# Performance work log

Hardware: AMD Instinct MI355X
Metric: run time of the kernel (lower is better)

Reference implementation:

```python
import jax, jax.numpy as jnp
import numpy as np

DIM = 2240; HEADS = 20; HD = 112
B = 1; F = 8; H = 16; W = 28; S = F * H * W; ENC = 300
HID = int(3.0 * DIM)  # 6720
EPS_LN = 1e-6; EPS_RMS = 1e-5


def setup_inputs():
    ks = iter(jax.random.split(jax.random.key(0), 64))
    nrm = lambda shape, s=1.0: jax.random.normal(next(ks), shape, jnp.float32) * s
    wsc = 0.02
    inp = dict(
        hidden_states=nrm((B, S, DIM)),
        encoder_hidden_states=nrm((B, ENC, DIM)),
        timestep=nrm((B, 6 * DIM), 0.1),
        freqs_cos=nrm((1, S, 1, HD)),
        freqs_sin=nrm((1, S, 1, HD)),
        scale_shift_table=nrm((6, DIM), 1.0 / np.sqrt(DIM)),
    )
    for p in ("a1", "a2"):
        inp[p + "_qw"] = nrm((DIM, DIM), wsc); inp[p + "_qb"] = jnp.zeros((DIM,), jnp.float32)
        inp[p + "_kw"] = nrm((DIM, DIM), wsc); inp[p + "_kb"] = jnp.zeros((DIM,), jnp.float32)
        inp[p + "_vw"] = nrm((DIM, DIM), wsc); inp[p + "_vb"] = jnp.zeros((DIM,), jnp.float32)
        inp[p + "_nq"] = jnp.ones((DIM,), jnp.float32)
        inp[p + "_nk"] = jnp.ones((DIM,), jnp.float32)
        inp[p + "_ow"] = nrm((DIM, DIM), wsc); inp[p + "_ob"] = jnp.zeros((DIM,), jnp.float32)
    inp["ff_inv_w"] = nrm((1, 1, DIM, 2 * HID), wsc)
    inp["ff_inv_b"] = jnp.zeros((2 * HID,), jnp.float32)
    inp["ff_depth_w"] = nrm((3, 3, 1, 2 * HID), wsc)
    inp["ff_depth_b"] = jnp.zeros((2 * HID,), jnp.float32)
    inp["ff_point_w"] = nrm((1, 1, HID, DIM), wsc)
    inp["ff_temp_w"] = nrm((3, 1, DIM, DIM), wsc)
    inp["frames"] = F; inp["height"] = H; inp["width"] = W
    return inp


def _ln(x):  # LayerNorm, no affine (elementwise_affine=False)
    m = jnp.mean(x, -1, keepdims=True)
    v = jnp.mean((x - m) ** 2, -1, keepdims=True)
    return (x - m) * jax.lax.rsqrt(v + EPS_LN)


def _rms(x, w):  # rms_norm_across_heads on full inner dim
    return x * jax.lax.rsqrt(jnp.mean(x * x, -1, keepdims=True) + EPS_RMS) * w


def _rope(x, cos, sin):  # interleaved rotary as in SanaLinearAttnProcessor3_0
    x1, x2 = x[..., 0::2], x[..., 1::2]
    c, s = cos[..., 0::2], sin[..., 1::2]
    out = jnp.stack([x1 * c - x2 * s, x1 * s + x2 * c], axis=-1)
    return out.reshape(x.shape)


def _conv(x, k, padding, groups=1):
    return jax.lax.conv_general_dilated(
        x, k, (1, 1), padding,
        dimension_numbers=("NHWC", "HWIO", "NHWC"),
        feature_group_count=groups)


def _linear_attn(x, qw, qb, kw, kb, vw, vb, nq, nk, ow, ob, cos, sin):
    b, s, _ = x.shape
    q = jax.nn.relu(_rms(x @ qw + qb, nq)).reshape(b, s, HEADS, HD)
    k = jax.nn.relu(_rms(x @ kw + kb, nk)).reshape(b, s, HEADS, HD)
    v = (x @ vw + vb).reshape(b, s, HEADS, HD)
    qr, kr = _rope(q, cos, sin), _rope(k, cos, sin)
    ksum = jnp.sum(k, axis=1)                             # [b,h,d] (un-rotated)
    denom = jnp.einsum("bhd,bshd->bsh", ksum, q) + 1e-15  # z^{-1}
    scores = jnp.einsum("bshe,bshd->bhed", v, kr)         # [b,h,dv,d]
    out = jnp.einsum("bhed,bshd->bshe", scores, qr) / denom[..., None]
    return out.reshape(b, s, HEADS * HD) @ ow + ob


def _cross_attn(x, enc, qw, qb, kw, kb, vw, vb, nq, nk, ow, ob):
    b, s, _ = x.shape; t = enc.shape[1]
    q = _rms(x @ qw + qb, nq).reshape(b, s, HEADS, HD)
    k = _rms(enc @ kw + kb, nk).reshape(b, t, HEADS, HD)
    v = (enc @ vw + vb).reshape(b, t, HEADS, HD)
    logits = jnp.einsum("bshd,bthd->bhst", q, k) / np.sqrt(HD).astype(np.float32)
    attn = jax.nn.softmax(logits, axis=-1)
    out = jnp.einsum("bhst,bthd->bshd", attn, v).reshape(b, s, HEADS * HD)
    return out @ ow + ob


def _ff(x, inv_w, inv_b, depth_w, depth_b, point_w, temp_w, f, h, w):
    b = x.shape[0]
    y = x.reshape(b * f, h, w, DIM)
    y = jax.nn.silu(_conv(y, inv_w, "SAME") + inv_b)
    y = _conv(y, depth_w, "SAME", groups=2 * HID) + depth_b
    a, g = y[..., :HID], y[..., HID:]
    y = _conv(a * jax.nn.silu(g), point_w, "SAME")        # [bf,h,w,DIM]
    yt = y.reshape(b, f, h * w, DIM)                      # conv over frames axis
    yt = yt + _conv(yt, temp_w, ((1, 1), (0, 0)))
    return yt.reshape(b, f, h, w, DIM)


def reference(hidden_states, encoder_hidden_states, timestep, freqs_cos, freqs_sin,
              scale_shift_table,
              a1_qw, a1_qb, a1_kw, a1_kb, a1_vw, a1_vb, a1_nq, a1_nk, a1_ow, a1_ob,
              a2_qw, a2_qb, a2_kw, a2_kb, a2_vw, a2_vb, a2_nq, a2_nk, a2_ow, a2_ob,
              ff_inv_w, ff_inv_b, ff_depth_w, ff_depth_b, ff_point_w, ff_temp_w,
              frames, height, width):
    b = hidden_states.shape[0]
    mods = scale_shift_table[None] + timestep.reshape(b, 6, DIM)
    sh_msa, sc_msa, g_msa, sh_mlp, sc_mlp, g_mlp = jnp.split(mods, 6, axis=1)
    nh = _ln(hidden_states) * (1 + sc_msa) + sh_msa
    attn = _linear_attn(nh, a1_qw, a1_qb, a1_kw, a1_kb, a1_vw, a1_vb,
                        a1_nq, a1_nk, a1_ow, a1_ob, freqs_cos, freqs_sin)
    x = hidden_states + g_msa * attn
    x = x + _cross_attn(x, encoder_hidden_states, a2_qw, a2_qb, a2_kw, a2_kb,
                        a2_vw, a2_vb, a2_nq, a2_nk, a2_ow, a2_ob)
    nh = _ln(x) * (1 + sc_mlp) + sh_mlp
    ff = _ff(nh.reshape(b, frames, height, width, DIM),
             ff_inv_w, ff_inv_b, ff_depth_w, ff_depth_b, ff_point_w, ff_temp_w,
             frames, height, width)
    x = x + g_mlp * ff.reshape(b, frames * height * width, DIM)
    return x
```

## Files before the change

kernel.cpp:

```cpp
#include <hip/hip_runtime.h>

#define DIMC 2240
#define STOK 3584
#define ENCT 300
#define NH   20
#define HDIM 112
#define HID1 6720
#define HID2 13440
#define DD   (2240*2240)
#define SD   (3584*2240)

typedef short bf16x8 __attribute__((ext_vector_type(8)));
typedef float f32x4  __attribute__((ext_vector_type(4)));

__device__ __forceinline__ unsigned short f2bf(float f){
  unsigned int u = __float_as_uint(f);
  u += 0x7fffu + ((u >> 16) & 1u);
  return (unsigned short)(u >> 16);
}
__device__ __forceinline__ float bf2f(unsigned short h){
  return __uint_as_float(((unsigned int)h) << 16);
}
__device__ __forceinline__ void gl_lds16(const unsigned short* g, unsigned short* l){
  __builtin_amdgcn_global_load_lds(
      (const __attribute__((address_space(1))) unsigned int*)(const void*)g,
      (__attribute__((address_space(3))) unsigned int*)(void*)l, 16, 0, 0);
}

__global__ void cvt_k(const float4* __restrict__ src, ushort4* __restrict__ dst, int n4){
  int i = blockIdx.x*256 + threadIdx.x;
  if (i < n4){
    float4 v = src[i];
    ushort4 o; o.x = f2bf(v.x); o.y = f2bf(v.y); o.z = f2bf(v.z); o.w = f2bf(v.w);
    dst[i] = o;
  }
}

__global__ __launch_bounds__(256) void cvt_t_k(const float* __restrict__ src,
    unsigned short* __restrict__ dst, int rows, int ldsrc, int c0, int nc){
  __shared__ float tile[32][33];
  const int tx = threadIdx.x & 31, ty = threadIdx.x >> 5;
  const int colBase = blockIdx.x*32;
  #pragma unroll
  for (int i = 0; i < 4; ++i){
    int rr = blockIdx.y*32 + ty + i*8;
    int cc = colBase + tx;
    tile[ty + i*8][tx] = (cc < nc) ? src[(size_t)rr*ldsrc + c0 + cc] : 0.f;
  }
  __syncthreads();
  #pragma unroll
  for (int i = 0; i < 4; ++i){
    int n = colBase + ty + i*8;
    int k = blockIdx.y*32 + tx;
    dst[(size_t)n*rows + k] = f2bf(tile[tx][ty + i*8]);
  }
}

__global__ void pack3_k(float* __restrict__ dst, const float* __restrict__ b0,
    const float* __restrict__ b1, const float* __restrict__ b2, int nslots){
  int i = blockIdx.x*256 + threadIdx.x;
  if (i >= nslots*2304) return;
  int slot = i / 2304, d = i - slot*2304;
  const float* src = (slot == 0) ? b0 : ((slot == 1) ? b1 : b2);
  dst[i] = (d < 2240) ? src[d] : 0.f;
}

__global__ void mods_k(const float* __restrict__ sst, const float* __restrict__ ts, float* __restrict__ mods){
  int i = blockIdx.x*256 + threadIdx.x;
  if (i < 6*DIMC) mods[i] = sst[i] + ts[i];
}

__global__ __launch_bounds__(256) void ln_mod_k(const float* __restrict__ x,
    const float* __restrict__ mods, int shj, int scj, unsigned short* __restrict__ out)
{
  const int s = blockIdx.x;
  const float4* row4 = reinterpret_cast<const float4*>(x + (size_t)s*DIMC);
  const float4* sh4 = reinterpret_cast<const float4*>(mods + shj*DIMC);
  const float4* sc4 = reinterpret_cast<const float4*>(mods + scj*DIMC);
  float sum = 0.f, sq = 0.f;
  for (int o = threadIdx.x; o < 560; o += 256){
    float4 v = row4[o];
    sum += v.x + v.y + v.z + v.w;
    sq  += v.x*v.x + v.y*v.y + v.z*v.z + v.w*v.w;
  }
  #pragma unroll
  for (int o = 32; o; o >>= 1){ sum += __shfl_down(sum, o); sq += __shfl_down(sq, o); }
  __shared__ float sA[4], sB[4];
  int w = threadIdx.x >> 6, l = threadIdx.x & 63;
  if (!l){ sA[w] = sum; sB[w] = sq; }
  __syncthreads();
  sum = sA[0]+sA[1]+sA[2]+sA[3];
  sq  = sB[0]+sB[1]+sB[2]+sB[3];
  float mean = sum * (1.f/DIMC);
  float rs = rsqrtf(sq*(1.f/DIMC) - mean*mean + 1e-6f);
  unsigned short* orow = out + (size_t)s*DIMC;
  for (int o = threadIdx.x; o < 560; o += 256){
    float4 v = row4[o], sc = sc4[o], sh = sh4[o];
    ushort4 r;
    r.x = f2bf((v.x-mean)*rs*(1.f + sc.x) + sh.x);
    r.y = f2bf((v.y-mean)*rs*(1.f + sc.y) + sh.y);
    r.z = f2bf((v.z-mean)*rs*(1.f + sc.z) + sh.z);
    r.w = f2bf((v.w-mean)*rs*(1.f + sc.w) + sh.w);
    *reinterpret_cast<ushort4*>(orow + o*4) = r;
  }
}

template<int RELU, int ROPE>
__global__ __launch_bounds__(256) void rms_bf_k(unsigned short* __restrict__ x, const float* __restrict__ nw,
    const float* __restrict__ cosb, const float* __restrict__ sinb, unsigned short* __restrict__ xr)
{
  const int s = blockIdx.x;
  unsigned short* row = x + (size_t)s*DIMC;
  float sq = 0.f;
  for (int o = threadIdx.x; o < 280; o += 256){
    uint4 v = *reinterpret_cast<const uint4*>(row + o*8);
    unsigned int uu[4] = {v.x, v.y, v.z, v.w};
    #pragma unroll
    for (int j = 0; j < 4; ++j){
      float lo = bf2f((unsigned short)(uu[j] & 0xffffu));
      float hi = bf2f((unsigned short)(uu[j] >> 16));
      sq += lo*lo + hi*hi;
    }
  }
  #pragma unroll
  for (int o = 32; o; o >>= 1) sq += __shfl_down(sq, o);
  __shared__ float sB[4];
  int w = threadIdx.x >> 6, l = threadIdx.x & 63;
  if (!l) sB[w] = sq;
  __syncthreads();
  sq = sB[0]+sB[1]+sB[2]+sB[3];
  float rs = rsqrtf(sq*(1.f/DIMC) + 1e-5f);
  for (int o = threadIdx.x; o < 280; o += 256){
    uint4 v = *reinterpret_cast<const uint4*>(row + o*8);
    unsigned int uu[4] = {v.x, v.y, v.z, v.w};
    float4 n0 = *reinterpret_cast<const float4*>(nw + o*8);
    float4 n1 = *reinterpret_cast<const float4*>(nw + o*8 + 4);
    float nn[8] = {n0.x,n0.y,n0.z,n0.w,n1.x,n1.y,n1.z,n1.w};
    float vals[8];
    #pragma unroll
    for (int j = 0; j < 4; ++j){
      vals[2*j]   = bf2f((unsigned short)(uu[j] & 0xffffu))*rs*nn[2*j];
      vals[2*j+1] = bf2f((unsigned short)(uu[j] >> 16))*rs*nn[2*j+1];
    }
    if constexpr (RELU){
      #pragma unroll
      for (int j = 0; j < 8; ++j) vals[j] = fmaxf(vals[j], 0.f);
    }
    uint4 o1;
    unsigned int* po = &o1.x;
    #pragma unroll
    for (int j = 0; j < 4; ++j)
      po[j] = (unsigned int)f2bf(vals[2*j]) | ((unsigned int)f2bf(vals[2*j+1]) << 16);
    *reinterpret_cast<uint4*>(row + o*8) = o1;
    if constexpr (ROPE){
      int jb = (o*8) % HDIM;
      uint4 o2;
      unsigned int* pr = &o2.x;
      #pragma unroll
      for (int p = 0; p < 4; ++p){
        float c  = cosb[(size_t)s*HDIM + jb + 2*p];
        float sn = sinb[(size_t)s*HDIM + jb + 2*p + 1];
        float r0 = vals[2*p]*c - vals[2*p+1]*sn;
        float r1 = vals[2*p]*sn + vals[2*p+1]*c;
        pr[p] = (unsigned int)f2bf(r0) | ((unsigned int)f2bf(r1) << 16);
      }
      *reinterpret_cast<uint4*>(xr + (size_t)s*DIMC + o*8) = o2;
    }
  }
}

template<int EPI>
__global__ __launch_bounds__(256) void gemm_bt(
  const unsigned short* __restrict__ A, const unsigned short* __restrict__ Bt,
  const float* __restrict__ bias, float* __restrict__ Cf, unsigned short* __restrict__ Cb,
  const float* __restrict__ res, const float* __restrict__ gate,
  int M, int N, int K, int ldc, int PW)
{
  __shared__ __align__(16) unsigned short Al[128*64];
  __shared__ __align__(16) unsigned short Bl[128*64];
  const int gx = gridDim.x, gy = gridDim.y;
  const int nwg = gx*gy;
  const int orig = blockIdx.y*gx + blockIdx.x;
  const int qq = nwg >> 3, rr = nwg & 7;
  const int xcd = orig & 7, li = orig >> 3;
  const int wg = (xcd < rr ? xcd*(qq+1) : rr*(qq+1) + (xcd-rr)*qq) + li;
  const int ppw = gy*PW;
  const int panel = wg / ppw, rm = wg - panel*ppw;
  const int mrow = rm / PW;
  const int m0 = mrow*128;
  const int n0 = (panel*PW + (rm - mrow*PW))*128;

  const int t = threadIdx.x, lane = t & 63, w = t >> 6;
  const int wr = w >> 1, wc = w & 1;
  const int l16 = lane & 15, lk = lane >> 4;

  const int lr8 = lane >> 3;
  const int sc  = (lane & 7) ^ lr8;
  const unsigned short* Aps[4];
  const unsigned short* Bps[4];
  #pragma unroll
  for (int i = 0; i < 4; ++i){
    int ar = m0 + w*32 + i*8 + lr8;
    int br = n0 + w*32 + i*8 + lr8;
    Aps[i] = A  + (size_t)min(ar, M-1)*K + sc*8;
    Bps[i] = Bt + (size_t)br*K + sc*8;
  }
  unsigned short* Ad = Al + w*2048;
  unsigned short* Bd = Bl + w*2048;

  f32x4 acc[4][4] = {};
  for (int k0 = 0; k0 < K; k0 += 64){
    __syncthreads();
    #pragma unroll
    for (int i = 0; i < 4; ++i){
      gl_lds16(Aps[i] + k0, Ad + i*512);
      gl_lds16(Bps[i] + k0, Bd + i*512);
    }
    __syncthreads();
    #pragma unroll
    for (int kk = 0; kk < 2; ++kk){
      bf16x8 af[4], bfr[4];
      const int chb = (kk*4 + lk) ^ (l16 & 7);
      #pragma unroll
      for (int m = 0; m < 4; ++m)
        af[m] = *reinterpret_cast<const bf16x8*>(Al + (wr*64 + m*16 + l16)*64 + chb*8);
      #pragma unroll
      for (int n = 0; n < 4; ++n)
        bfr[n] = *reinterpret_cast<const bf16x8*>(Bl + (wc*64 + n*16 + l16)*64 + chb*8);
      #pragma unroll
      for (int m = 0; m < 4; ++m)
        #pragma unroll
        for (int n = 0; n < 4; ++n)
          acc[m][n] = __builtin_amdgcn_mfma_f32_16x16x32_bf16(af[m], bfr[n], acc[m][n], 0, 0, 0);
    }
  }

  const int rb = m0 + wr*64 + lk*4;
  const int cb = n0 + wc*64 + l16;
  #pragma unroll
  for (int m = 0; m < 4; ++m){
    #pragma unroll
    for (int r = 0; r < 4; ++r){
      int row = rb + m*16 + r;
      if (row >= M) continue;
      #pragma unroll
      for (int n = 0; n < 4; ++n){
        int col = cb + n*16;
        if (col >= N) continue;
        float v = acc[m][n][r];
        float bv = bias ? bias[col] : 0.f;
        if constexpr (EPI == 6){
          int slot = col / 2304;
          int d = col - slot*2304;
          if (d < 2240)
            Cb[(size_t)slot*ldc + (size_t)row*2240 + d] = f2bf(v + bv);
        } else {
          size_t idx = (size_t)row*ldc + col;
          if constexpr (EPI == 0){ Cf[idx] = v + bv; }
          else if constexpr (EPI == 1){ float u = v + bv; Cb[idx] = f2bf(u / (1.f + __expf(-u))); }
          else if constexpr (EPI == 2){ Cb[idx] = f2bf(v + bv); }
          else if constexpr (EPI == 3){ float u = res[idx] + gate[col]*(v + bv); Cf[idx] = u; Cb[idx] = f2bf(u); }
          else if constexpr (EPI == 4){ Cf[idx] = res[idx] + v + bv; }
          else { Cf[idx] += v; }
        }
      }
    }
  }
}

__global__ void colsum_k(const unsigned short* __restrict__ k, float* __restrict__ kpart){
  int d = blockIdx.x*256 + threadIdx.x;
  if (d >= DIMC) return;
  int ch = blockIdx.y, s0 = ch*128;
  float acc = 0.f;
  for (int s = s0; s < s0+128; ++s) acc += bf2f(k[(size_t)s*DIMC + d]);
  kpart[(size_t)ch*DIMC + d] = acc;
}
__global__ void ksumred_k(const float* __restrict__ kpart, float* __restrict__ ksum){
  int d = blockIdx.x*256 + threadIdx.x;
  if (d >= DIMC) return;
  float a = 0.f;
  for (int c = 0; c < 28; ++c) a += kpart[(size_t)c*DIMC + d];
  ksum[d] = a;
}
__global__ __launch_bounds__(256) void denom_k(const unsigned short* __restrict__ q,
    const float* __restrict__ ksum, float* __restrict__ denom)
{
  int s = blockIdx.x; int w = threadIdx.x >> 6, l = threadIdx.x & 63;
  for (int h = w; h < NH; h += 4){
    const unsigned short* qb = q + (size_t)s*DIMC + h*HDIM;
    const float* kb = ksum + h*HDIM;
    float v = bf2f(qb[l])*kb[l];
    if (l < 48) v += bf2f(qb[64+l])*kb[64+l];
    #pragma unroll
    for (int o = 32; o; o >>= 1) v += __shfl_down(v, o);
    if (!l) denom[s*NH + h] = v + 1e-15f;
  }
}

#define SLSC 136
__device__ __forceinline__ int sc_idx(int e, int s){
  return e*SLSC + (s ^ (((e >> 3) & 7) << 3));
}
__global__ __launch_bounds__(256) void scores_k(const unsigned short* __restrict__ v,
    const unsigned short* __restrict__ kr, float* __restrict__ part)
{
  const int h = blockIdx.x, ch = blockIdx.y;
  __shared__ __align__(16) unsigned short Vt[112*SLSC];
  __shared__ __align__(16) unsigned short Kt[112*SLSC];
  const int t = threadIdx.x, lane = t & 63, w = t >> 6;
  const int l16 = lane & 15, lk = lane >> 4;
  const int sbase = ch*128;

  for (int p = t; p < 1792; p += 256){
    int s = p / 14, oc = (p % 14) * 8;
    bf16x8 vv = *reinterpret_cast<const bf16x8*>(v  + (size_t)(sbase+s)*DIMC + h*HDIM + oc);
    bf16x8 kk = *reinterpret_cast<const bf16x8*>(kr + (size_t)(sbase+s)*DIMC + h*HDIM + oc);
    #pragma unroll
    for (int j = 0; j < 8; ++j){
      Vt[sc_idx(oc+j, s)] = (unsigned short)vv[j];
      Kt[sc_idx(oc+j, s)] = (unsigned short)kk[j];
    }
  }
  __syncthreads();

  f32x4 acc[2][7] = {};
  #pragma unroll
  for (int ks = 0; ks < 4; ++ks){
    const int sf = ks*32 + lk*8;
    bf16x8 bfrg[7];
    #pragma unroll
    for (int nt = 0; nt < 7; ++nt){
      int d = nt*16 + l16;
      bfrg[nt] = *reinterpret_cast<const bf16x8*>(&Kt[d*SLSC + (sf ^ (((d >> 3) & 7) << 3))]);
    }
    #pragma unroll
    for (int mi = 0; mi < 2; ++mi){
      int mt = w + mi*4;
      if (mt < 7){
        int e = mt*16 + l16;
        bf16x8 afrg = *reinterpret_cast<const bf16x8*>(&Vt[e*SLSC + (sf ^ (((e >> 3) & 7) << 3))]);
        #pragma unroll
        for (int nt = 0; nt < 7; ++nt)
          acc[mi][nt] = __builtin_amdgcn_mfma_f32_16x16x32_bf16(afrg, bfrg[nt], acc[mi][nt], 0, 0, 0);
      }
    }
  }

  float* pout = part + ((size_t)ch*NH + h)*12544;
  #pragma unroll
  for (int mi = 0; mi < 2; ++mi){
    int mt = w + mi*4;
    if (mt >= 7) continue;
    #pragma unroll
    for (int nt = 0; nt < 7; ++nt)
      #pragma unroll
      for (int r = 0; r < 4; ++r)
        pout[(size_t)(mt*16 + lk*4 + r)*HDIM + nt*16 + l16] = acc[mi][nt][r];
  }
}
__global__ void scred_k(const float* __restrict__ part, unsigned short* __restrict__ sc){
  int i = blockIdx.x*256 + threadIdx.x;
  if (i >= NH*HDIM*HDIM) return;
  float a = 0.f;
  #pragma unroll
  for (int c = 0; c < 28; ++c) a += part[(size_t)c*(NH*HDIM*HDIM) + i];
  sc[i] = f2bf(a);
}

__global__ __launch_bounds__(256) void linout_k(const unsigned short* __restrict__ qr,
    const unsigned short* __restrict__ scores, const float* __restrict__ denom,
    unsigned short* __restrict__ out)
{
  const int h = blockIdx.y;
  const int t = threadIdx.x, lane = t & 63, w = t >> 6;
  const int l16 = lane & 15, lk = lane >> 4;
  const int s0 = blockIdx.x*64 + w*16;
  const unsigned short* qrow = qr + (size_t)(s0 + l16)*DIMC + h*HDIM;
  const unsigned short* sb = scores + (size_t)h*12544;
  f32x4 acc[7] = {};
  #pragma unroll
  for (int ks = 0; ks < 4; ++ks){
    int d0 = ks*32 + lk*8;
    bf16x8 a = {};
    if (d0 < HDIM) a = *reinterpret_cast<const bf16x8*>(qrow + d0);
    #pragma unroll
    for (int nt = 0; nt < 7; ++nt){
      bf16x8 b = {};
      if (d0 < HDIM) b = *reinterpret_cast<const bf16x8*>(sb + (size_t)(nt*16 + l16)*HDIM + d0);
      acc[nt] = __builtin_amdgcn_mfma_f32_16x16x32_bf16(a, b, acc[nt], 0, 0, 0);
    }
  }
  #pragma unroll
  for (int r = 0; r < 4; ++r){
    int s = s0 + lk*4 + r;
    float dn = 1.f / denom[(size_t)s*NH + h];
    #pragma unroll
    for (int nt = 0; nt < 7; ++nt)
      out[(size_t)s*DIMC + h*HDIM + nt*16 + l16] = f2bf(acc[nt][r]*dn);
  }
}

__global__ __launch_bounds__(256) void xattn_k(
    const unsigned short* __restrict__ q,
    const unsigned short* __restrict__ k2,
    const unsigned short* __restrict__ v2,
    unsigned short* __restrict__ outb)
{
  const int h = blockIdx.y;
  const int w = threadIdx.x >> 6, lane = threadIdx.x & 63;
  const int l16 = lane & 15, lk = lane >> 4;
  const float scale = 0.09449111825230679f;

  __shared__ __align__(16) unsigned short Kl[64][136];
  __shared__ __align__(16) unsigned short Vl[112][72];
  __shared__ __align__(16) unsigned short Pl[4][16][72];

  bf16x8 qf[4];
  const unsigned short* qbase = q + (size_t)(blockIdx.x*64 + w*16 + l16)*DIMC + h*HDIM;
  #pragma unroll
  for (int c = 0; c < 4; ++c){
    int d0 = c*32 + lk*8;
    bf16x8 z = {};
    qf[c] = (d0 < HDIM) ? *reinterpret_cast<const bf16x8*>(qbase + d0) : z;
  }

  f32x4 lg[5][4] = {};
  #pragma unroll
  for (int c = 0; c < 5; ++c){
    const int kbase = c*64;
    const int nk = (c == 4) ? (ENCT - 256) : 64;
    __syncthreads();
    #pragma unroll
    for (int it = 0; it < 4; ++it){
      int li = it*256 + threadIdx.x;
      int key = li >> 4, d0 = (li & 15) << 3;
      uint4 val = make_uint4(0u,0u,0u,0u);
      if (key < nk && d0 < HDIM)
        val = *reinterpret_cast<const uint4*>(k2 + (size_t)(kbase+key)*DIMC + h*HDIM + d0);
      *reinterpret_cast<uint4*>(&Kl[key][d0]) = val;
    }
    __syncthreads();
    #pragma unroll
    for (int nt = 0; nt < 4; ++nt){
      #pragma unroll
      for (int ks = 0; ks < 4; ++ks){
        bf16x8 kf = *reinterpret_cast<const bf16x8*>(&Kl[nt*16 + l16][ks*32 + lk*8]);
        lg[c][nt] = __builtin_amdgcn_mfma_f32_16x16x32_bf16(qf[ks], kf, lg[c][nt], 0, 0, 0);
      }
    }
  }

  float mx[4] = {-3e38f, -3e38f, -3e38f, -3e38f};
  #pragma unroll
  for (int c = 0; c < 5; ++c)
    #pragma unroll
    for (int nt = 0; nt < 4; ++nt){
      bool valid = (c*64 + nt*16 + l16) < ENCT;
      #pragma unroll
      for (int r = 0; r < 4; ++r){
        float v = valid ? lg[c][nt][r]*scale : -3e38f;
        lg[c][nt][r] = v;
        mx[r] = fmaxf(mx[r], v);
      }
    }
  #pragma unroll
  for (int o = 1; o < 16; o <<= 1)
    #pragma unroll
    for (int r = 0; r < 4; ++r) mx[r] = fmaxf(mx[r], __shfl_xor(mx[r], o));
  float sm[4] = {0.f, 0.f, 0.f, 0.f};
  #pragma unroll
  for (int c = 0; c < 5; ++c)
    #pragma unroll
    for (int nt = 0; nt < 4; ++nt)
      #pragma unroll
      for (int r = 0; r < 4; ++r){
        float e = __expf(lg[c][nt][r] - mx[r]);
        lg[c][nt][r] = e;
        sm[r] += e;
      }
  #pragma unroll
  for (int o = 1; o < 16; o <<= 1)
    #pragma unroll
    for (int r = 0; r < 4; ++r) sm[r] += __shfl_xor(sm[r], o);
  float inv[4];
  #pragma unroll
  for (int r = 0; r < 4; ++r) inv[r] = 1.f / sm[r];

  f32x4 oacc[7] = {};
  #pragma unroll
  for (int c = 0; c < 5; ++c){
    const int kbase = c*64;
    const int nk = (c == 4) ? (ENCT - 256) : 64;
    __syncthreads();
    #pragma unroll
    for (int it = 0; it < 4; ++it){
      int li = it*256 + threadIdx.x;
      if (li < 896){
        int key = li/14, d0 = (li%14)*8;
        if (key < nk){
          bf16x8 vv = *reinterpret_cast<const bf16x8*>(v2 + (size_t)(kbase+key)*DIMC + h*HDIM + d0);
          #pragma unroll
          for (int j = 0; j < 8; ++j) Vl[d0+j][key] = (unsigned short)vv[j];
        } else {
          #pragma unroll
          for (int j = 0; j < 8; ++j) Vl[d0+j][key] = 0;
        }
      }
    }
    #pragma unroll
    for (int nt = 0; nt < 4; ++nt)
      #pragma unroll
      for (int r = 0; r < 4; ++r)
        Pl[w][lk*4 + r][nt*16 + l16] = f2bf(lg[c][nt][r]);
    __syncthreads();
    #pragma unroll
    for (int ks = 0; ks < 2; ++ks){
      bf16x8 pf = *reinterpret_cast<const bf16x8*>(&Pl[w][l16][ks*32 + lk*8]);
      #pragma unroll
      for (int n = 0; n < 7; ++n){
        bf16x8 vf = *reinterpret_cast<const bf16x8*>(&Vl[n*16 + l16][ks*32 + lk*8]);
        oacc[n] = __builtin_amdgcn_mfma_f32_16x16x32_bf16(pf, vf, oacc[n], 0, 0, 0);
      }
    }
  }

  const int orow = blockIdx.x*64 + w*16 + lk*4;
  #pragma unroll
  for (int n = 0; n < 7; ++n)
    #pragma unroll
    for (int r = 0; r < 4; ++r)
      outb[(size_t)(orow + r)*DIMC + h*HDIM + n*16 + l16] = f2bf(oacc[n][r]*inv[r]);
}

__global__ __launch_bounds__(256) void dw_k(const unsigned short* __restrict__ y1,
    const float* __restrict__ dw, const float* __restrict__ db, unsigned short* __restrict__ y2)
{
  int c = (blockIdx.y*256 + threadIdx.x)*2;
  if (c >= HID1) return;
  int bx = blockIdx.x;
  int xp = bx % 14;
  int yt = (bx / 14) & 3;
  int f  = bx / 56;
  int x0 = xp*2, y0 = yt*4;

  float wa[9][2], wg[9][2];
  #pragma unroll
  for (int tp = 0; tp < 9; ++tp){
    float2 va = *reinterpret_cast<const float2*>(dw + tp*HID2 + c);
    float2 vg = *reinterpret_cast<const float2*>(dw + tp*HID2 + c + HID1);
    wa[tp][0] = va.x; wa[tp][1] = va.y;
    wg[tp][0] = vg.x; wg[tp][1] = vg.y;
  }
  float2 ba = *reinterpret_cast<const float2*>(db + c);
  float2 bg = *reinterpret_cast<const float2*>(db + c + HID1);
  float a[4][2][2], g[4][2][2];
  #pragma unroll
  for (int r = 0; r < 4; ++r)
    #pragma unroll
    for (int cc = 0; cc < 2; ++cc){
      a[r][cc][0] = ba.x; a[r][cc][1] = ba.y;
      g[r][cc][0] = bg.x; g[r][cc][1] = bg.y;
    }

  #pragma unroll
  for (int dy6 = 0; dy6 < 6; ++dy6){
    int y = y0 - 1 + dy6;
    if ((unsigned)y >= 16u) continue;
    #pragma unroll
    for (int dxc = 0; dxc < 4; ++dxc){
      int x = x0 - 1 + dxc;
      if ((unsigned)x >= 28u) continue;
      size_t base = ((size_t)(f*16 + y)*28 + x)*HID2;
      unsigned int a01 = *reinterpret_cast<const unsigned int*>(y1 + base + c);
      unsigned int g01 = *reinterpret_cast<const unsigned int*>(y1 + base + c + HID1);
      float fa0 = bf2f((unsigned short)(a01 & 0xffffu));
      float fa1 = bf2f((unsigned short)(a01 >> 16));
      float fg0 = bf2f((unsigned short)(g01 & 0xffffu));
      float fg1 = bf2f((unsigned short)(g01 >> 16));
      #pragma unroll
      for (int r = 0; r < 4; ++r){
        int kdy = dy6 - r;
        if (kdy < 0 || kdy > 2) continue;
        #pragma unroll
        for (int cc = 0; cc < 2; ++cc){
          int kdx = dxc - cc;
          if (kdx < 0 || kdx > 2) continue;
          int tp = kdy*3 + kdx;
          a[r][cc][0] += fa0*wa[tp][0]; a[r][cc][1] += fa1*wa[tp][1];
          g[r][cc][0] += fg0*wg[tp][0]; g[r][cc][1] += fg1*wg[tp][1];
        }
      }
    }
  }
  #pragma unroll
  for (int r = 0; r < 4; ++r)
    #pragma unroll
    for (int cc = 0; cc < 2; ++cc){
      float s0 = g[r][cc][0] / (1.f + __expf(-g[r][cc][0]));
      float s1 = g[r][cc][1] / (1.f + __expf(-g[r][cc][1]));
      int pos = (f*16 + y0 + r)*28 + x0 + cc;
      unsigned int o = (unsigned int)f2bf(a[r][cc][0]*s0) | ((unsigned int)f2bf(a[r][cc][1]*s1) << 16);
      *reinterpret_cast<unsigned int*>(y2 + (size_t)pos*HID1 + c) = o;
    }
}

__global__ void final_k(const float* __restrict__ x2, const unsigned short* __restrict__ y3,
    const float* __restrict__ tc, const float* __restrict__ mods, float* __restrict__ out)
{
  int i4 = (blockIdx.x*256 + threadIdx.x)*4;
  if (i4 >= SD) return;
  int d = i4 % DIMC;
  float4 xv = *reinterpret_cast<const float4*>(x2 + i4);
  float4 tv = *reinterpret_cast<const float4*>(tc + i4);
  float4 gv = *reinterpret_cast<const float4*>(mods + 5*DIMC + d);
  ushort4 yv = *reinterpret_cast<const ushort4*>(y3 + i4);
  float4 o;
  o.x = xv.x + gv.x*(bf2f(yv.x) + tv.x);
  o.y = xv.y + gv.y*(bf2f(yv.y) + tv.y);
  o.z = xv.z + gv.z*(bf2f(yv.z) + tv.z);
  o.w = xv.w + gv.w*(bf2f(yv.w) + tv.w);
  *reinterpret_cast<float4*>(out + i4) = o;
}

extern "C" void kernel_launch(void* const* d_in, const int* in_sizes, int n_in,
                              void* d_out, int out_size, void* d_ws, size_t ws_size,
                              hipStream_t stream)
{
  const float* hid   = (const float*)d_in[0];
  const float* enc   = (const float*)d_in[1];
  const float* tstep = (const float*)d_in[2];
  const float* fcos  = (const float*)d_in[3];
  const float* fsin  = (const float*)d_in[4];
  const float* sst   = (const float*)d_in[5];
  const float *a1_qw=(const float*)d_in[6],  *a1_qb=(const float*)d_in[7];
  const float *a1_kw=(const float*)d_in[8],  *a1_kb=(const float*)d_in[9];
  const float *a1_vw=(const float*)d_in[10], *a1_vb=(const float*)d_in[11];
  const float *a1_nq=(const float*)d_in[12], *a1_nk=(const float*)d_in[13];
  const float *a1_ow=(const float*)d_in[14], *a1_ob=(const float*)d_in[15];
  const float *a2_qw=(const float*)d_in[16], *a2_qb=(const float*)d_in[17];
  const float *a2_kw=(const float*)d_in[18], *a2_kb=(const float*)d_in[19];
  const float *a2_vw=(const float*)d_in[20], *a2_vb=(const float*)d_in[21];
  const float *a2_nq=(const float*)d_in[22], *a2_nk=(const float*)d_in[23];
  const float *a2_ow=(const float*)d_in[24], *a2_ob=(const float*)d_in[25];
  const float *ff_inv_w=(const float*)d_in[26], *ff_inv_b=(const float*)d_in[27];
  const float *ff_dw=(const float*)d_in[28], *ff_db=(const float*)d_in[29];
  const float *ff_pw=(const float*)d_in[30];
  const float *ff_tw=(const float*)d_in[31];
  float* out = (float*)d_out;

  const size_t SLOTB = (size_t)SD*2;
  char* ws = (char*)d_ws;
  size_t off = 0;
  auto alloc = [&](size_t n){ void* p = ws + off; off += (n + 255) & ~(size_t)255; return p; };

  char* P = (char*)alloc(6*SLOTB);
  float* x1    = (float*)alloc((size_t)SD*4);
  unsigned short* nh2b = (unsigned short*)alloc(SLOTB);
  float* x2    = (float*)alloc((size_t)SD*4);
  unsigned short* k2b = (unsigned short*)alloc((size_t)ENCT*DIMC*2);
  unsigned short* v2b = (unsigned short*)alloc((size_t)ENCT*DIMC*2);
  unsigned short* encb = (unsigned short*)alloc((size_t)ENCT*DIMC*2);
  float* modsb = (float*)alloc(6*DIMC*4);
  float* ksum  = (float*)alloc(DIMC*4);
  float* kpart = (float*)alloc((size_t)28*DIMC*4);
  float* denom = (float*)alloc((size_t)STOK*NH*4);
  unsigned short* scorb = (unsigned short*)alloc((size_t)NH*HDIM*HDIM*2);
  float* bias3 = (float*)alloc(3*2304*4);
  unsigned short* Wbig = (unsigned short*)alloc((size_t)6912*DIMC*2);

  unsigned short* P0 = (unsigned short*)P;
  unsigned short* P1 = (unsigned short*)(P + 1*SLOTB);
  unsigned short* P2 = (unsigned short*)(P + 2*SLOTB);
  unsigned short* P3 = (unsigned short*)(P + 3*SLOTB);
  unsigned short* P4 = (unsigned short*)(P + 4*SLOTB);
  unsigned short* P5 = (unsigned short*)(P + 5*SLOTB);
  unsigned short* nhb = P0;
  unsigned short* y1b = P0;
  unsigned short* y2b = (unsigned short*)x1;
  unsigned short* y3b = P0;
  float* tc = (float*)(P + 1*SLOTB);
  float* spart = (float*)P1;

  auto cvt = [&](const float* s, unsigned short* d, size_t n){
    int n4 = (int)(n/4);
    cvt_k<<<dim3((n4+255)/256), 256, 0, stream>>>((const float4*)s, (ushort4*)d, n4);
  };
  auto cvtT = [&](const float* s, unsigned short* d, int rows, int ldsrc, int c0, int nc, int ncPad){
    cvt_t_k<<<dim3(ncPad/32, rows/32), 256, 0, stream>>>(s, d, rows, ldsrc, c0, nc);
  };
  auto gemm_grid = [&](int M, int Npad){ return dim3(Npad/128, (M+127)/128); };

  mods_k<<<dim3((6*DIMC+255)/256), 256, 0, stream>>>(sst, tstep, modsb);
  cvt(enc, encb, (size_t)ENCT*DIMC);

  ln_mod_k<<<dim3(STOK), 256, 0, stream>>>(hid, modsb, 0, 1, nhb);
  pack3_k<<<dim3((3*2304+255)/256), 256, 0, stream>>>(bias3, a1_qb, a1_kb, a1_vb, 3);
  cvtT(a1_qw, Wbig + (size_t)0*2304*DIMC, DIMC, DIMC, 0, DIMC, 2304);
  cvtT(a1_kw, Wbig + (size_t)1*2304*DIMC, DIMC, DIMC, 0, DIMC, 2304);
  cvtT(a1_vw, Wbig + (size_t)2*2304*DIMC, DIMC, DIMC, 0, DIMC, 2304);
  gemm_bt<6><<<gemm_grid(STOK, 6912), 256, 0, stream>>>(nhb, Wbig, bias3, nullptr, P1,
                                                        nullptr, nullptr, STOK, 6912, DIMC, SD, 6);
  rms_bf_k<1,1><<<dim3(STOK), 256, 0, stream>>>(P1, a1_nq, fcos, fsin, P4);
  rms_bf_k<1,1><<<dim3(STOK), 256, 0, stream>>>(P2, a1_nk, fcos, fsin, P5);
  colsum_k<<<dim3(9, 28), 256, 0, stream>>>(P2, kpart);
  ksumred_k<<<dim3(9), 256, 0, stream>>>(kpart, ksum);
  denom_k<<<dim3(STOK), 256, 0, stream>>>(P1, ksum, denom);
  scores_k<<<dim3(NH, 28), 256, 0, stream>>>(P3, P5, spart);
  scred_k<<<dim3((NH*HDIM*HDIM+255)/256), 256, 0, stream>>>(spart, scorb);
  linout_k<<<dim3(STOK/64, NH), 256, 0, stream>>>(P4, scorb, denom, P1);
  dim3 gMN = gemm_grid(STOK, 2304);
  cvtT(a1_ow, Wbig, DIMC, DIMC, 0, DIMC, 2304);
  gemm_bt<3><<<gMN, 256, 0, stream>>>(P1, Wbig, a1_ob, x1, P2, hid, modsb + 2*DIMC, STOK, DIMC, DIMC, DIMC, 6);

  cvtT(a2_qw, Wbig, DIMC, DIMC, 0, DIMC, 2304);
  gemm_bt<2><<<gMN, 256, 0, stream>>>(P2, Wbig, a2_qb, nullptr, P3, nullptr, nullptr, STOK, DIMC, DIMC, DIMC, 6);
  pack3_k<<<dim3((2*2304+255)/256), 256, 0, stream>>>(bias3, a2_kb, a2_vb, a2_vb, 2);
  cvtT(a2_kw, Wbig + (size_t)0*2304*DIMC, DIMC, DIMC, 0, DIMC, 2304);
  cvtT(a2_vw, Wbig + (size_t)1*2304*DIMC, DIMC, DIMC, 0, DIMC, 2304);
  gemm_bt<6><<<gemm_grid(ENCT, 4608), 256, 0, stream>>>(encb, Wbig, bias3, nullptr, k2b,
                                                        nullptr, nullptr, ENCT, 4608, DIMC, ENCT*DIMC, 6);
  rms_bf_k<0,0><<<dim3(STOK), 256, 0, stream>>>(P3, a2_nq, nullptr, nullptr, nullptr);
  rms_bf_k<0,0><<<dim3(ENCT), 256, 0, stream>>>(k2b, a2_nk, nullptr, nullptr, nullptr);
  xattn_k<<<dim3(STOK/64, NH), 256, 0, stream>>>(P3, k2b, v2b, P4);
  cvtT(a2_ow, Wbig, DIMC, DIMC, 0, DIMC, 2304);
  gemm_bt<4><<<gMN, 256, 0, stream>>>(P4, Wbig, a2_ob, x2, nullptr, x1, nullptr, STOK, DIMC, DIMC, DIMC, 6);

  ln_mod_k<<<dim3(STOK), 256, 0, stream>>>(x2, modsb, 3, 4, nh2b);
  for (int q = 0; q < 2; ++q){
    int c0 = q*6720;
    cvtT(ff_inv_w, Wbig, DIMC, HID2, c0, 6720, 6912);
    gemm_bt<1><<<gemm_grid(STOK, 6912), 256, 0, stream>>>(nh2b, Wbig, ff_inv_b + c0, nullptr, y1b + c0,
                                                          nullptr, nullptr, STOK, 6720, DIMC, HID2, 6);
  }
  dw_k<<<dim3(448, 14), 256, 0, stream>>>(y1b, ff_dw, ff_db, y2b);
  cvtT(ff_pw, Wbig, HID1, DIMC, 0, DIMC, 2304);
  gemm_bt<2><<<gMN, 256, 0, stream>>>(y2b, Wbig, nullptr, nullptr, y3b,
                                      nullptr, nullptr, STOK, DIMC, HID1, DIMC, 2);
  cvtT(ff_tw + (size_t)DD, Wbig, DIMC, DIMC, 0, DIMC, 2304);
  gemm_bt<0><<<gMN, 256, 0, stream>>>(y3b, Wbig, nullptr, tc, nullptr, nullptr, nullptr, STOK, DIMC, DIMC, DIMC, 6);
  dim3 gT = gemm_grid(3136, 2304);
  cvtT(ff_tw, Wbig, DIMC, DIMC, 0, DIMC, 2304);
  gemm_bt<5><<<gT, 256, 0, stream>>>(y3b, Wbig, nullptr, tc + (size_t)448*DIMC, nullptr, nullptr, nullptr, 3136, DIMC, DIMC, DIMC, 6);
  cvtT(ff_tw + (size_t)2*DD, Wbig, DIMC, DIMC, 0, DIMC, 2304);
  gemm_bt<5><<<gT, 256, 0, stream>>>(y3b + (size_t)448*DIMC, Wbig, nullptr, tc, nullptr, nullptr, nullptr, 3136, DIMC, DIMC, DIMC, 6);

  final_k<<<dim3((SD/4+255)/256), 256, 0, stream>>>(x2, y3b, tc, modsb, out);
}
```

Before: 1.486 ms.

## Fuse temporal conv taps into one K-concatenated GEMM with zero-padded input

Replaces the three separate temporal-conv GEMMs (one full plus two accumulate-into-shifted-rows) with a single GEMM of K=6720. The A pointer is shifted by one frame per K-section, and the input is zero-padded by a frame on each side so the boundary frames read zeros. The weight transposes are also batched into one launch over blockIdx.z. This removes two read-modify-write passes over the fp32 accumulator and several launches, at the cost of a padding kernel and a larger bf16 staging buffer.

```diff
diff --git a/kernel.cpp b/kernel.cpp
--- a/kernel.cpp
+++ b/kernel.cpp
@@ -36,8 +36,12 @@
   }
 }
 
-__global__ __launch_bounds__(256) void cvt_t_k(const float* __restrict__ src,
-    unsigned short* __restrict__ dst, int rows, int ldsrc, int c0, int nc){
+__global__ __launch_bounds__(256) void cvtT3_k(const float* __restrict__ s0,
+    const float* __restrict__ s1, const float* __restrict__ s2,
+    unsigned short* __restrict__ dst, int rows, int ldsrc, int c0, int nc,
+    int ldd, long long dzoff){
+  const float* src = (blockIdx.z == 0) ? s0 : ((blockIdx.z == 1) ? s1 : s2);
+  unsigned short* d = dst + (size_t)blockIdx.z * (size_t)dzoff;
   __shared__ float tile[32][33];
   const int tx = threadIdx.x & 31, ty = threadIdx.x >> 5;
   const int colBase = blockIdx.x*32;
@@ -52,7 +56,15 @@
   for (int i = 0; i < 4; ++i){
     int n = colBase + ty + i*8;
     int k = blockIdx.y*32 + tx;
-    dst[(size_t)n*rows + k] = f2bf(tile[tx][ty + i*8]);
+    d[(size_t)n*ldd + k] = f2bf(tile[tx][ty + i*8]);
+  }
+}
+
+__global__ void zpad_k(unsigned short* __restrict__ m0, unsigned short* __restrict__ m1){
+  int i = blockIdx.x*256 + threadIdx.x;
+  if (i < 125440){
+    reinterpret_cast<uint4*>(m0)[i] = make_uint4(0u,0u,0u,0u);
+    reinterpret_cast<uint4*>(m1)[i] = make_uint4(0u,0u,0u,0u);
   }
 }
 
@@ -174,7 +186,7 @@
   const unsigned short* __restrict__ A, const unsigned short* __restrict__ Bt,
   const float* __restrict__ bias, float* __restrict__ Cf, unsigned short* __restrict__ Cb,
   const float* __restrict__ res, const float* __restrict__ gate,
-  int M, int N, int K, int ldc, int PW)
+  int M, int N, int K, int ldc, int PW, int lda, int tcsh)
 {
   __shared__ __align__(16) unsigned short Al[128*64];
   __shared__ __align__(16) unsigned short Bl[128*64];
@@ -202,7 +214,7 @@
   for (int i = 0; i < 4; ++i){
     int ar = m0 + w*32 + i*8 + lr8;
     int br = n0 + w*32 + i*8 + lr8;
-    Aps[i] = A  + (size_t)min(ar, M-1)*K + sc*8;
+    Aps[i] = A  + (size_t)min(ar, M-1)*lda + sc*8;
     Bps[i] = Bt + (size_t)br*K + sc*8;
   }
   unsigned short* Ad = Al + w*2048;
@@ -210,11 +222,18 @@
 
   f32x4 acc[4][4] = {};
   for (int k0 = 0; k0 < K; k0 += 64){
+    size_t aoff;
+    if (tcsh){
+      int sec = (k0 >= 4480) ? 2 : ((k0 >= 2240) ? 1 : 0);
+      aoff = (size_t)(sec*448)*lda + (unsigned)(k0 - sec*2240);
+    } else {
+      aoff = (size_t)k0;
+    }
     __syncthreads();
     #pragma unroll
     for (int i = 0; i < 4; ++i){
-      gl_lds16(Aps[i] + k0, Ad + i*512);
-      gl_lds16(Bps[i] + k0, Bd + i*512);
+      gl_lds16(Aps[i] + aoff, Ad + i*512);
+      gl_lds16(Bps[i] + k0,   Bd + i*512);
     }
     __syncthreads();
     #pragma unroll
@@ -678,16 +697,18 @@
   unsigned short* nhb = P0;
   unsigned short* y1b = P0;
   unsigned short* y2b = (unsigned short*)x1;
-  unsigned short* y3b = P0;
-  float* tc = (float*)(P + 1*SLOTB);
+  unsigned short* y3pad = P0;
+  unsigned short* y3  = y3pad + (size_t)448*DIMC;
+  float* tc = (float*)(P + 2*SLOTB);
   float* spart = (float*)P1;
 
   auto cvt = [&](const float* s, unsigned short* d, size_t n){
     int n4 = (int)(n/4);
     cvt_k<<<dim3((n4+255)/256), 256, 0, stream>>>((const float4*)s, (ushort4*)d, n4);
   };
-  auto cvtT = [&](const float* s, unsigned short* d, int rows, int ldsrc, int c0, int nc, int ncPad){
-    cvt_t_k<<<dim3(ncPad/32, rows/32), 256, 0, stream>>>(s, d, rows, ldsrc, c0, nc);
+  auto cvtT3 = [&](const float* s0, const float* s1, const float* s2, unsigned short* d,
+                   int rows, int ldsrc, int c0, int nc, int ncPad, int ldd, long long dzoff, int nz){
+    cvtT3_k<<<dim3(ncPad/32, rows/32, nz), 256, 0, stream>>>(s0, s1, s2, d, rows, ldsrc, c0, nc, ldd, dzoff);
   };
   auto gemm_grid = [&](int M, int Npad){ return dim3(Npad/128, (M+127)/128); };
 
@@ -696,11 +717,9 @@
 
   ln_mod_k<<<dim3(STOK), 256, 0, stream>>>(hid, modsb, 0, 1, nhb);
   pack3_k<<<dim3((3*2304+255)/256), 256, 0, stream>>>(bias3, a1_qb, a1_kb, a1_vb, 3);
-  cvtT(a1_qw, Wbig + (size_t)0*2304*DIMC, DIMC, DIMC, 0, DIMC, 2304);
-  cvtT(a1_kw, Wbig + (size_t)1*2304*DIMC, DIMC, DIMC, 0, DIMC, 2304);
-  cvtT(a1_vw, Wbig + (size_t)2*2304*DIMC, DIMC, DIMC, 0, DIMC, 2304);
+  cvtT3(a1_qw, a1_kw, a1_vw, Wbig, DIMC, DIMC, 0, DIMC, 2304, DIMC, (long long)2304*DIMC, 3);
   gemm_bt<6><<<gemm_grid(STOK, 6912), 256, 0, stream>>>(nhb, Wbig, bias3, nullptr, P1,
-                                                        nullptr, nullptr, STOK, 6912, DIMC, SD, 6);
+                                                        nullptr, nullptr, STOK, 6912, DIMC, SD, 6, DIMC, 0);
   rms_bf_k<1,1><<<dim3(STOK), 256, 0, stream>>>(P1, a1_nq, fcos, fsin, P4);
   rms_bf_k<1,1><<<dim3(STOK), 256, 0, stream>>>(P2, a1_nk, fcos, fsin, P5);
   colsum_k<<<dim3(9, 28), 256, 0, stream>>>(P2, kpart);
@@ -710,40 +729,37 @@
   scred_k<<<dim3((NH*HDIM*HDIM+255)/256), 256, 0, stream>>>(spart, scorb);
   linout_k<<<dim3(STOK/64, NH), 256, 0, stream>>>(P4, scorb, denom, P1);
   dim3 gMN = gemm_grid(STOK, 2304);
-  cvtT(a1_ow, Wbig, DIMC, DIMC, 0, DIMC, 2304);
-  gemm_bt<3><<<gMN, 256, 0, stream>>>(P1, Wbig, a1_ob, x1, P2, hid, modsb + 2*DIMC, STOK, DIMC, DIMC, DIMC, 6);
-
-  cvtT(a2_qw, Wbig, DIMC, DIMC, 0, DIMC, 2304);
-  gemm_bt<2><<<gMN, 256, 0, stream>>>(P2, Wbig, a2_qb, nullptr, P3, nullptr, nullptr, STOK, DIMC, DIMC, DIMC, 6);
+  cvtT3(a1_ow, a1_ow, a1_ow, Wbig, DIMC, DIMC, 0, DIMC, 2304, DIMC, 0, 1);
+  gemm_bt<3><<<gMN, 256, 0, stream>>>(P1, Wbig, a1_ob, x1, P2, hid, modsb + 2*DIMC, STOK, DIMC, DIMC, DIMC, 6, DIMC, 0);
+
+  cvtT3(a2_qw, a2_qw, a2_qw, Wbig, DIMC, DIMC, 0, DIMC, 2304, DIMC, 0, 1);
+  gemm_bt<2><<<gMN, 256, 0, stream>>>(P2, Wbig, a2_qb, nullptr, P3, nullptr, nullptr, STOK, DIMC, DIMC, DIMC, 6, DIMC, 0);
   pack3_k<<<dim3((2*2304+255)/256), 256, 0, stream>>>(bias3, a2_kb, a2_vb, a2_vb, 2);
-  cvtT(a2_kw, Wbig + (size_t)0*2304*DIMC, DIMC, DIMC, 0, DIMC, 2304);
-  cvtT(a2_vw, Wbig + (size_t)1*2304*DIMC, DIMC, DIMC, 0, DIMC, 2304);
+  cvtT3(a2_kw, a2_vw, a2_vw, Wbig, DIMC, DIMC, 0, DIMC, 2304, DIMC, (long long)2304*DIMC, 2);
   gemm_bt<6><<<gemm_grid(ENCT, 4608), 256, 0, stream>>>(encb, Wbig, bias3, nullptr, k2b,
-                                                        nullptr, nullptr, ENCT, 4608, DIMC, ENCT*DIMC, 6);
+                                                        nullptr, nullptr, ENCT, 4608, DIMC, ENCT*DIMC, 6, DIMC, 0);
   rms_bf_k<0,0><<<dim3(STOK), 256, 0, stream>>>(P3, a2_nq, nullptr, nullptr, nullptr);
   rms_bf_k<0,0><<<dim3(ENCT), 256, 0, stream>>>(k2b, a2_nk, nullptr, nullptr, nullptr);
   xattn_k<<<dim3(STOK/64, NH), 256, 0, stream>>>(P3, k2b, v2b, P4);
-  cvtT(a2_ow, Wbig, DIMC, DIMC, 0, DIMC, 2304);
-  gemm_bt<4><<<gMN, 256, 0, stream>>>(P4, Wbig, a2_ob, x2, nullptr, x1, nullptr, STOK, DIMC, DIMC, DIMC, 6);
+  cvtT3(a2_ow, a2_ow, a2_ow, Wbig, DIMC, DIMC, 0, DIMC, 2304, DIMC, 0, 1);
+  gemm_bt<4><<<gMN, 256, 0, stream>>>(P4, Wbig, a2_ob, x2, nullptr, x1, nullptr, STOK, DIMC, DIMC, DIMC, 6, DIMC, 0);
 
   ln_mod_k<<<dim3(STOK), 256, 0, stream>>>(x2, modsb, 3, 4, nh2b);
   for (int q = 0; q < 2; ++q){
     int c0 = q*6720;
-    cvtT(ff_inv_w, Wbig, DIMC, HID2, c0, 6720, 6912);
+    cvtT3(ff_inv_w, ff_inv_w, ff_inv_w, Wbig, DIMC, HID2, c0, 6720, 6912, DIMC, 0, 1);
     gemm_bt<1><<<gemm_grid(STOK, 6912), 256, 0, stream>>>(nh2b, Wbig, ff_inv_b + c0, nullptr, y1b + c0,
-                                                          nullptr, nullptr, STOK, 6720, DIMC, HID2, 6);
+                                                          nullptr, nullptr, STOK, 6720, DIMC, HID2, 6, DIMC, 0);
   }
   dw_k<<<dim3(448, 14), 256, 0, stream>>>(y1b, ff_dw, ff_db, y2b);
-  cvtT(ff_pw, Wbig, HID1, DIMC, 0, DIMC, 2304);
-  gemm_bt<2><<<gMN, 256, 0, stream>>>(y2b, Wbig, nullptr, nullptr, y3b,
-                                      nullptr, nullptr, STOK, DIMC, HID1, DIMC, 2);
-  cvtT(ff_tw + (size_t)DD, Wbig, DIMC, DIMC, 0, DIMC, 2304);
-  gemm_bt<0><<<gMN, 256, 0, stream>>>(y3b, Wbig, nullptr, tc, nullptr, nullptr, nullptr, STOK, DIMC, DIMC, DIMC, 6);
-  dim3 gT = gemm_grid(3136, 2304);
-  cvtT(ff_tw, Wbig, DIMC, DIMC, 0, DIMC, 2304);
-  gemm_bt<5><<<gT, 256, 0, stream>>>(y3b, Wbig, nullptr, tc + (size_t)448*DIMC, nullptr, nullptr, nullptr, 3136, DIMC, DIMC, DIMC, 6);
-  cvtT(ff_tw + (size_t)2*DD, Wbig, DIMC, DIMC, 0, DIMC, 2304);
-  gemm_bt<5><<<gT, 256, 0, stream>>>(y3b + (size_t)448*DIMC, Wbig, nullptr, tc, nullptr, nullptr, nullptr, 3136, DIMC, DIMC, DIMC, 6);
-
-  final_k<<<dim3((SD/4+255)/256), 256, 0, stream>>>(x2, y3b, tc, modsb, out);
-}
+  zpad_k<<<dim3(490), 256, 0, stream>>>(y3pad, y3pad + (size_t)(448 + STOK)*DIMC);
+  cvtT3(ff_pw, ff_pw, ff_pw, Wbig, HID1, DIMC, 0, DIMC, 2304, HID1, 0, 1);
+  gemm_bt<2><<<gMN, 256, 0, stream>>>(y2b, Wbig, nullptr, nullptr, y3,
+                                      nullptr, nullptr, STOK, DIMC, HID1, DIMC, 2, HID1, 0);
+  cvtT3(ff_tw, ff_tw + (size_t)DD, ff_tw + (size_t)2*DD, Wbig,
+        DIMC, DIMC, 0, DIMC, 2304, 6720, 2240LL, 3);
+  gemm_bt<0><<<gMN, 256, 0, stream>>>(y3pad, Wbig, nullptr, tc, nullptr, nullptr, nullptr,
+                                      STOK, DIMC, 6720, DIMC, 6, DIMC, 1);
+
+  final_k<<<dim3((SD/4+255)/256), 256, 0, stream>>>(x2, y3, tc, modsb, out);
+}
```

Result: faster. 1.360 ms (-8.5%).
